# Performance work log

Measured on AMD Instinct MI355X. Metric: run time of the kernel, lower is better.

## Reference

```python
import jax, jax.numpy as jnp
import numpy as np

B, S, C = 32, 512, 384
MAX_LEN = 4096
MAX_DUR = 16


def setup_inputs() -> dict:
    key = jax.random.key(0)
    kx, kd = jax.random.split(key)
    x = jax.random.normal(kx, (B, S, C), dtype=jnp.float32)
    durations = jax.random.randint(kd, (B, S), 0, MAX_DUR, dtype=jnp.int32)
    return {"x": x, "durations": durations, "max_length": MAX_LEN}


def reference(x, durations, max_length):
    # Round (no-op for int durations, kept for faithfulness to torch.round().long())
    d = jnp.round(durations.astype(jnp.float32)).astype(jnp.int32)  # [B, S]
    # _limit_durations is equivalent to clipping the cumulative sum at max_length:
    # the first token crossing max_length gets truncated, all later tokens zeroed.
    ends = jnp.clip(jnp.cumsum(d, axis=1), 0, max_length)          # [B, S]
    total = ends[:, -1]                                            # [B]
    t = jnp.arange(max_length, dtype=jnp.int32)                    # [T]
    # frame t belongs to phoneme j where starts[j] <= t < ends[j];
    # searchsorted(ends, t, 'right') skips zero-duration tokens automatically.
    idx = jax.vmap(lambda e: jnp.searchsorted(e, t, side='right'))(ends)  # [B, T]
    mel_masks = t[None, :] >= total[:, None]                       # [B, T] True = pad
    idx_c = jnp.clip(idx, 0, x.shape[1] - 1)
    expanded = jnp.take_along_axis(x, idx_c[:, :, None], axis=1)   # [B, T, C]
    expanded = jnp.where(mel_masks[:, :, None], jnp.zeros((), x.dtype), expanded)
    return expanded, mel_masks
```

## Files before the change

kernel.cpp:

```cpp
#include <hip/hip_runtime.h>

#define BATCH 32
#define SEQ 512
#define CH 384
#define MAXL 4096
#define CH4 (CH / 4)

__global__ __launch_bounds__(SEQ) void lr_scan_kernel(
    const int* __restrict__ durations,
    const int* __restrict__ max_len_p,
    int* __restrict__ ws_idx,
    float* __restrict__ out_mask)
{
    __shared__ int s_cum[SEQ];
    __shared__ int s_idx[MAXL];

    const int tid = threadIdx.x;
    const int b = blockIdx.x;
    const int maxlen = max_len_p[0];

    s_cum[tid] = durations[b * SEQ + tid];
    __syncthreads();
    #pragma unroll
    for (int off = 1; off < SEQ; off <<= 1) {
        int v = (tid >= off) ? s_cum[tid - off] : 0;
        __syncthreads();
        s_cum[tid] += v;
        __syncthreads();
    }

    for (int t = tid; t < MAXL; t += SEQ) s_idx[t] = -1;
    __syncthreads();

    int e = min(s_cum[tid], maxlen);
    int st = (tid == 0) ? 0 : min(s_cum[tid - 1], maxlen);
    e = min(e, MAXL);
    st = min(st, MAXL);
    for (int t = st; t < e; ++t) s_idx[t] = tid;
    __syncthreads();

    for (int t = tid; t < MAXL; t += SEQ) {
        int v = s_idx[t];
        ws_idx[b * MAXL + t] = v;
        out_mask[b * MAXL + t] = (v < 0) ? 1.0f : 0.0f;
    }
}

__global__ __launch_bounds__(256) void lr_expand_kernel(
    const float4* __restrict__ x,
    const int* __restrict__ ws_idx,
    float4* __restrict__ out)
{
    const int r0 = blockIdx.x * 8;
    #pragma unroll
    for (int k = 0; k < 3; ++k) {
        int local = threadIdx.x + k * 256;
        int lr = local / CH4;
        int c4 = local - lr * CH4;
        int r = r0 + lr;
        int idx = ws_idx[r];
        float4 v = make_float4(0.f, 0.f, 0.f, 0.f);
        if (idx >= 0) {
            int b = r >> 12;
            v = x[(b * SEQ + idx) * CH4 + c4];
        }
        out[(size_t)r * CH4 + c4] = v;
    }
}

extern "C" void kernel_launch(void* const* d_in, const int* in_sizes, int n_in,
                              void* d_out, int out_size, void* d_ws, size_t ws_size,
                              hipStream_t stream) {
    const float* x = (const float*)d_in[0];
    const int* durations = (const int*)d_in[1];
    const int* max_len_p = (const int*)d_in[2];
    float* out = (float*)d_out;
    float* out_mask = out + (size_t)BATCH * MAXL * CH;
    int* ws_idx = (int*)d_ws;

    lr_scan_kernel<<<BATCH, SEQ, 0, stream>>>(durations, max_len_p, ws_idx, out_mask);
    lr_expand_kernel<<<(BATCH * MAXL) / 8, 256, 0, stream>>>(
        (const float4*)x, ws_idx, (float4*)out);
}
```

Before: 224.6 us.

## Fuse scan and expand into one kernel with per-block binary search

Merges the duration scan and the gather-expand kernels into a single launch. Each block redundantly recomputes the per-batch prefix sum (two durations per thread) and binary-searches the index for its 32 output rows, so the workspace index round trip and the second launch go away. Output writes use nontemporal stores to avoid polluting the cache. The cost is redundant scan work in every block (4096 blocks each scanning 512 durations) plus extra syncs before the copy loop.

```diff
diff --git a/kernel.cpp b/kernel.cpp
--- a/kernel.cpp
+++ b/kernel.cpp
@@ -4,81 +4,84 @@
 #define SEQ 512
 #define CH 384
 #define MAXL 4096
-#define CH4 (CH / 4)
+#define CH4 96
+#define ROWS 32
+#define THREADS 256
+#define NT (ROWS * CH4)
 
-__global__ __launch_bounds__(SEQ) void lr_scan_kernel(
-    const int* __restrict__ durations,
+typedef float v4f __attribute__((ext_vector_type(4)));
+
+__global__ __launch_bounds__(THREADS) void lr_fused_kernel(
+    const v4f* __restrict__ x,
+    const int2* __restrict__ dur2,
     const int* __restrict__ max_len_p,
-    int* __restrict__ ws_idx,
+    v4f* __restrict__ out,
     float* __restrict__ out_mask)
 {
-    __shared__ int s_cum[SEQ];
-    __shared__ int s_idx[MAXL];
+    __shared__ int s_scan[THREADS];
+    __shared__ int s_end[SEQ];
+    __shared__ int s_idx[ROWS];
 
     const int tid = threadIdx.x;
-    const int b = blockIdx.x;
+    const int r0 = blockIdx.x * ROWS;
+    const int b  = r0 >> 12;
+    const int t0 = r0 & (MAXL - 1);
     const int maxlen = max_len_p[0];
 
-    s_cum[tid] = durations[b * SEQ + tid];
+    int2 d = dur2[b * (SEQ / 2) + tid];
+    s_scan[tid] = d.x + d.y;
     __syncthreads();
     #pragma unroll
-    for (int off = 1; off < SEQ; off <<= 1) {
-        int v = (tid >= off) ? s_cum[tid - off] : 0;
+    for (int off = 1; off < THREADS; off <<= 1) {
+        int v = (tid >= off) ? s_scan[tid - off] : 0;
         __syncthreads();
-        s_cum[tid] += v;
+        s_scan[tid] += v;
         __syncthreads();
     }
-
-    for (int t = tid; t < MAXL; t += SEQ) s_idx[t] = -1;
+    int incl = s_scan[tid];
+    s_end[2 * tid]     = min(incl - d.y, maxlen);
+    s_end[2 * tid + 1] = min(incl, maxlen);
     __syncthreads();
 
-    int e = min(s_cum[tid], maxlen);
-    int st = (tid == 0) ? 0 : min(s_cum[tid - 1], maxlen);
-    e = min(e, MAXL);
-    st = min(st, MAXL);
-    for (int t = st; t < e; ++t) s_idx[t] = tid;
+    const int total = s_end[SEQ - 1];
+
+    if (tid < ROWS) {
+        int t = t0 + tid;
+        int lo = 0, hi = SEQ;
+        #pragma unroll
+        for (int it = 0; it < 10; ++it) {
+            int mid = (lo + hi) >> 1;
+            if (s_end[mid] <= t) lo = mid + 1; else hi = mid;
+        }
+        bool masked = (t >= total);
+        s_idx[tid] = masked ? -1 : min(lo, SEQ - 1);
+        out_mask[r0 + tid] = masked ? 1.0f : 0.0f;
+    }
     __syncthreads();
 
-    for (int t = tid; t < MAXL; t += SEQ) {
-        int v = s_idx[t];
-        ws_idx[b * MAXL + t] = v;
-        out_mask[b * MAXL + t] = (v < 0) ? 1.0f : 0.0f;
-    }
-}
-
-__global__ __launch_bounds__(256) void lr_expand_kernel(
-    const float4* __restrict__ x,
-    const int* __restrict__ ws_idx,
-    float4* __restrict__ out)
-{
-    const int r0 = blockIdx.x * 8;
+    const v4f* xb = x + (size_t)b * SEQ * CH4;
+    v4f* ob = out + (size_t)r0 * CH4;
     #pragma unroll
-    for (int k = 0; k < 3; ++k) {
-        int local = threadIdx.x + k * 256;
+    for (int k = 0; k < NT / THREADS; ++k) {
+        int local = tid + k * THREADS;
         int lr = local / CH4;
         int c4 = local - lr * CH4;
-        int r = r0 + lr;
-        int idx = ws_idx[r];
-        float4 v = make_float4(0.f, 0.f, 0.f, 0.f);
-        if (idx >= 0) {
-            int b = r >> 12;
-            v = x[(b * SEQ + idx) * CH4 + c4];
-        }
-        out[(size_t)r * CH4 + c4] = v;
+        int idx = s_idx[lr];
+        v4f v = (v4f){0.f, 0.f, 0.f, 0.f};
+        if (idx >= 0) v = xb[idx * CH4 + c4];
+        __builtin_nontemporal_store(v, &ob[local]);
     }
 }
 
 extern "C" void kernel_launch(void* const* d_in, const int* in_sizes, int n_in,
                               void* d_out, int out_size, void* d_ws, size_t ws_size,
                               hipStream_t stream) {
-    const float* x = (const float*)d_in[0];
-    const int* durations = (const int*)d_in[1];
+    const v4f* x = (const v4f*)d_in[0];
+    const int2* dur2 = (const int2*)d_in[1];
     const int* max_len_p = (const int*)d_in[2];
     float* out = (float*)d_out;
     float* out_mask = out + (size_t)BATCH * MAXL * CH;
-    int* ws_idx = (int*)d_ws;
 
-    lr_scan_kernel<<<BATCH, SEQ, 0, stream>>>(durations, max_len_p, ws_idx, out_mask);
-    lr_expand_kernel<<<(BATCH * MAXL) / 8, 256, 0, stream>>>(
-        (const float4*)x, ws_idx, (float4*)out);
+    lr_fused_kernel<<<(BATCH * MAXL) / ROWS, THREADS, 0, stream>>>(
+        x, dur2, max_len_p, (v4f*)out, out_mask);
 }
```

Result: slower. 237.2 us (+5.6%).
